# Kernel optimization log

Hardware: AMD Instinct MI355X
Metric: run time of the kernel (lower is better)

Reference implementation:

```python
import jax, jax.numpy as jnp
import numpy as np

B, N, D, H = 1, 4096, 1024, 16
E = D // H  # head_dim = 64


def setup_inputs() -> dict:
    key = jax.random.key(0)
    ks = jax.random.split(key, 5)
    s = 0.02
    return {
        "query": jax.random.normal(ks[0], (B, N, D), dtype=jnp.float32),
        "Wq": jax.random.normal(ks[1], (D, D), dtype=jnp.float32) * s,
        "Wk": jax.random.normal(ks[2], (D, D), dtype=jnp.float32) * s,
        "Wv": jax.random.normal(ks[3], (D, D), dtype=jnp.float32) * s,
        "Wo": jax.random.normal(ks[4], (D, D), dtype=jnp.float32) * s,
        "bo": jnp.zeros((D,), dtype=jnp.float32),
    }


def reference(query, Wq, Wk, Wv, Wo, bo):
    # self-attention: key = value = query
    # nn.Linear: y = x @ W.T  (weights stored as [out, in])
    q = query @ Wq.T  # [b, n, d]
    k = query @ Wk.T
    v = query @ Wv.T
    # 'b n (h e) -> b h n e'
    q = q.reshape(B, N, H, E).transpose(0, 2, 1, 3)
    k = k.reshape(B, N, H, E).transpose(0, 2, 1, 3)
    v = v.reshape(B, N, H, E).transpose(0, 2, 1, 3)
    scale = 1.0 / jnp.sqrt(jnp.asarray(E, dtype=q.dtype))
    attn = jnp.einsum('bhne,bhme->bhnm', q, k) * scale  # [b, h, n, n]
    attn = jax.nn.softmax(attn, axis=-1)
    out = jnp.einsum('bhnm,bhme->bhne', attn, v)  # [b, h, n, e]
    # 'b h n e -> b n (h e)'
    out = out.transpose(0, 2, 1, 3).reshape(B, N, D)
    out = out @ Wo.T + bo
    return out
```

## Files before the change

kernel.cpp:

```cpp
#include <hip/hip_runtime.h>


typedef __attribute__((ext_vector_type(8))) __bf16 bf16x8;
typedef __attribute__((ext_vector_type(4))) float f32x4;
typedef __attribute__((ext_vector_type(16))) float f32x16;
typedef __attribute__((ext_vector_type(4))) unsigned short us4;
typedef __attribute__((ext_vector_type(4))) unsigned int u32x4;
typedef __attribute__((ext_vector_type(2))) unsigned int u32x2;

#define DEV __device__ __forceinline__

#define QSCALE 0.1803368801111204f

DEV unsigned short f2bf(float x) {
  union { float f; unsigned u; } c; c.f = x;
  unsigned u = c.u;
  u += 0x7FFFu + ((u >> 16) & 1u);
  return (unsigned short)(u >> 16);
}

DEV float expq(float x) {
#if __has_builtin(__builtin_amdgcn_exp2f)
  return __builtin_amdgcn_exp2f(x);
#else
  float r;
  asm("v_exp_f32 %0, %1" : "=v"(r) : "v"(x));
  return r;
#endif
}

DEV unsigned cvtpk_bf16(float lo, float hi) {
  unsigned r;
  asm("v_cvt_pk_bf16_f32 %0, %1, %2" : "=v"(r) : "v"(lo), "v"(hi));
  return r;
}

DEV void plswap_u(unsigned& a, unsigned& b) {
#if __has_builtin(__builtin_amdgcn_permlane32_swap)
  u32x2 r = __builtin_amdgcn_permlane32_swap(a, b, false, false);
  a = r.x; b = r.y;
#else
  asm("v_permlane32_swap_b32 %0, %1" : "+v"(a), "+v"(b));
#endif
}

DEV void plswap_f(float& a, float& b) {
  unsigned ua = __float_as_uint(a), ub = __float_as_uint(b);
  plswap_u(ua, ub);
  a = __uint_as_float(ua); b = __uint_as_float(ub);
}

DEV void gload16(const void* g, void* lds) {
  __builtin_amdgcn_global_load_lds(
      (const __attribute__((address_space(1))) unsigned int*)g,
      (__attribute__((address_space(3))) unsigned int*)lds, 16, 0, 0);
}

__global__ void cast_all(const float* __restrict__ q,
                         const float* __restrict__ wa,
                         const float* __restrict__ wb,
                         const float* __restrict__ wc,
                         const float* __restrict__ wd,
                         unsigned short* __restrict__ qo,
                         unsigned short* __restrict__ wout) {
  const int y = blockIdx.y;
  const int i = blockIdx.x * 256 + threadIdx.x;
  const float* src;
  unsigned short* dst;
  if (y < 4) {
    src = q + (size_t)y * 1048576;
    dst = qo + (size_t)y * 1048576;
  } else {
    src = (y == 4) ? wa : (y == 5) ? wb : (y == 6) ? wc : wd;
    dst = wout + (size_t)(y - 4) * 1048576;
  }
  float4 v = reinterpret_cast<const float4*>(src)[i];
  us4 o;
  o.x = f2bf(v.x); o.y = f2bf(v.y); o.z = f2bf(v.z); o.w = f2bf(v.w);
  reinterpret_cast<us4*>(dst)[i] = o;
}

__global__ __launch_bounds__(256)
void gemm_qkv(const unsigned short* __restrict__ A,
              const unsigned short* __restrict__ B,
              unsigned short* __restrict__ Qo,
              unsigned short* __restrict__ Ko,
              unsigned short* __restrict__ Vo) {
  constexpr int K = 1024, BK = 64;
  __shared__ unsigned short As[128 * BK];
  __shared__ unsigned short Bs[128 * BK];
  const int t = threadIdx.x;
  const int w = t >> 6, l = t & 63;
  const int brow = blockIdx.x * 128;
  const int bcol = blockIdx.y * 128;
  const int wr = w >> 1, wc = w & 1;
  const int lr = l >> 3;
  const int lc = ((l & 7) ^ lr) * 8;
  const int fr = l & 15;
  const int fcb = (l >> 4) * 16;
  const int swz = (l & 7) << 4;

  f32x4 acc[4][4] = {};
  const char* Asb = (const char*)As;
  const char* Bsb = (const char*)Bs;

  for (int k0 = 0; k0 < K; k0 += BK) {
#pragma unroll
    for (int i = 0; i < 4; ++i) {
      const int r = w * 32 + i * 8;
      gload16(A + (size_t)(brow + r + lr) * K + k0 + lc, (void*)(As + r * BK));
      gload16(B + (size_t)(bcol + r + lr) * K + k0 + lc, (void*)(Bs + r * BK));
    }
    __syncthreads();
#pragma unroll
    for (int kk = 0; kk < 2; ++kk) {
      bf16x8 af[4], bfr[4];
#pragma unroll
      for (int m = 0; m < 4; ++m)
        af[m] = *(const bf16x8*)(Asb + (wr * 64 + m * 16 + fr) * 128 +
                                 ((kk * 64 + fcb) ^ swz));
#pragma unroll
      for (int n = 0; n < 4; ++n)
        bfr[n] = *(const bf16x8*)(Bsb + (wc * 64 + n * 16 + fr) * 128 +
                                  ((kk * 64 + fcb) ^ swz));
#pragma unroll
      for (int m = 0; m < 4; ++m)
#pragma unroll
        for (int n = 0; n < 4; ++n)
          acc[m][n] = __builtin_amdgcn_mfma_f32_16x16x32_bf16(
              af[m], bfr[n], acc[m][n], 0, 0, 0);
    }
    __syncthreads();
  }

  const int seg = blockIdx.y >> 3;
  const int orow = brow + wr * 64 + (l >> 4) * 4;
  const int ocol = (blockIdx.y & 7) * 128 + wc * 64 + fr;
  if (seg == 1) {
#pragma unroll
    for (int n = 0; n < 4; ++n) {
      const int C = ocol + n * 16;
      const int bn = (C >> 6) * 262144 + ((C & 63) >> 3) * 512 + (C & 7);
#pragma unroll
      for (int m = 0; m < 4; ++m)
#pragma unroll
        for (int j = 0; j < 4; ++j) {
          const int R = orow + m * 16 + j;
          Ko[bn + (R >> 6) * 4096 + (R & 63) * 8] = f2bf(acc[m][n][j]);
        }
    }
  } else if (seg == 2) {
#pragma unroll
    for (int n = 0; n < 4; ++n) {
      const int C = ocol + n * 16;
      const int bn = (C >> 6) * 262144 + (C & 63) * 8;
#pragma unroll
      for (int m = 0; m < 4; ++m)
#pragma unroll
        for (int j = 0; j < 4; ++j) {
          const int R = orow + m * 16 + j;
          Vo[bn + (R >> 6) * 4096 + ((R & 63) >> 3) * 512 + (R & 7)] =
              f2bf(acc[m][n][j]);
        }
    }
  } else {
#pragma unroll
    for (int m = 0; m < 4; ++m)
#pragma unroll
      for (int n = 0; n < 4; ++n)
#pragma unroll
        for (int j = 0; j < 4; ++j)
          Qo[(size_t)(orow + m * 16 + j) * 1024 + (ocol + n * 16)] =
              f2bf(acc[m][n][j] * QSCALE);
  }
}

__global__ __launch_bounds__(256)
void gemm_out64(const unsigned short* __restrict__ A,
                const unsigned short* __restrict__ B,
                float* __restrict__ C, const float* __restrict__ bias) {
  constexpr int N = 1024, K = 1024, BK = 64;
  __shared__ unsigned short As[64 * BK];
  __shared__ unsigned short Bs[128 * BK];
  const int t = threadIdx.x;
  const int w = t >> 6, l = t & 63;
  const int brow = blockIdx.x * 64;
  const int bcol = blockIdx.y * 128;
  const int wr = w >> 1, wc = w & 1;
  const int lr = l >> 3;
  const int lc = ((l & 7) ^ lr) * 8;
  const int fr = l & 15;
  const int fcb = (l >> 4) * 16;
  const int swz = (l & 7) << 4;

  f32x4 acc[2][4] = {};
  const char* Asb = (const char*)As;
  const char* Bsb = (const char*)Bs;

  for (int k0 = 0; k0 < K; k0 += BK) {
#pragma unroll
    for (int i = 0; i < 2; ++i) {
      const int r = w * 16 + i * 8;
      gload16(A + (size_t)(brow + r + lr) * K + k0 + lc, (void*)(As + r * BK));
    }
#pragma unroll
    for (int i = 0; i < 4; ++i) {
      const int r = w * 32 + i * 8;
      gload16(B + (size_t)(bcol + r + lr) * K + k0 + lc, (void*)(Bs + r * BK));
    }
    __syncthreads();
#pragma unroll
    for (int kk = 0; kk < 2; ++kk) {
      bf16x8 af[2], bfr[4];
#pragma unroll
      for (int m = 0; m < 2; ++m)
        af[m] = *(const bf16x8*)(Asb + (wr * 32 + m * 16 + fr) * 128 +
                                 ((kk * 64 + fcb) ^ swz));
#pragma unroll
      for (int n = 0; n < 4; ++n)
        bfr[n] = *(const bf16x8*)(Bsb + (wc * 64 + n * 16 + fr) * 128 +
                                  ((kk * 64 + fcb) ^ swz));
#pragma unroll
      for (int m = 0; m < 2; ++m)
#pragma unroll
        for (int n = 0; n < 4; ++n)
          acc[m][n] = __builtin_amdgcn_mfma_f32_16x16x32_bf16(
              af[m], bfr[n], acc[m][n], 0, 0, 0);
    }
    __syncthreads();
  }

  const int orow = brow + wr * 32 + (l >> 4) * 4;
  const int ocol = bcol + wc * 64 + fr;
#pragma unroll
  for (int m = 0; m < 2; ++m)
#pragma unroll
    for (int n = 0; n < 4; ++n)
#pragma unroll
      for (int j = 0; j < 4; ++j)
        C[(size_t)(orow + m * 16 + j) * N + (ocol + n * 16)] =
            acc[m][n][j] + bias[ocol + n * 16];
}

__global__ __launch_bounds__(512, 4)
void attn_v14(const unsigned short* __restrict__ Q,
              const unsigned short* __restrict__ Kp,
              const unsigned short* __restrict__ Vp,
              unsigned short* __restrict__ AO) {
  constexpr int D = 1024, NIT = 32;
  __shared__ unsigned long long LDSA[65536 / 8];
  char* LDS = (char*)LDSA;
  const int t = threadIdx.x, w = t >> 6, l = t & 63;
  const int g = w >> 2, wg = w & 3;
  const int flat = blockIdx.x;
  const int c = flat & 7, ii = flat >> 3;
  const int h = c * 2 + (ii >> 5);
  const int qt = ii & 31;
  const int q0 = qt * 128 + wg * 32;
  const int ln = l & 31, hi = l >> 5;
  const int lr = l >> 3;
  const int ko = hi * 1024 + ln * 16;

  char* kb0 = LDS + (g * 2 + 0) * 8192;
  char* kb1 = LDS + (g * 2 + 1) * 8192;
  char* vb0 = LDS + 32768 + (g * 2 + 0) * 8192;
  char* vb1 = LDS + 32768 + (g * 2 + 1) * 8192;

  bf16x8 qf[4];
  {
    const unsigned short* qp = Q + (size_t)(q0 + ln) * D + h * 64 + hi * 8;
#pragma unroll
    for (int ks = 0; ks < 4; ++ks) qf[ks] = *(const bf16x8*)(qp + ks * 16);
  }

  f32x16 oacc0 = {}, oacc1 = {};
  float lsum = 0.f;

  const int stoff = wg * 2048;
  const char* Kg = (const char*)Kp + ((size_t)(h * 64 + g)) * 8192 + stoff + l * 16;
  const char* Vg = (const char*)Vp + ((size_t)(h * 64 + g)) * 8192 + stoff + l * 16;

  auto stage = [&](char* kd, char* vd, int it) {
    const size_t o = (size_t)it * 16384;
    gload16(Kg + o, kd + stoff);
    gload16(Kg + o + 1024, kd + stoff + 1024);
    gload16(Vg + o, vd + stoff);
    gload16(Vg + o + 1024, vd + stoff + 1024);
  };

  stage(kb0, vb0, 0);
  __syncthreads();

  for (int i = 0; i < NIT; ++i) {
    const char* ksb = (i & 1) ? kb1 : kb0;
    const char* vsb = (i & 1) ? vb1 : vb0;
    if (i + 1 < NIT)
      stage((i & 1) ? kb0 : kb1, (i & 1) ? vb0 : vb1, i + 1);

    f32x16 sa = {}, sb = {};
    __builtin_amdgcn_s_setprio(1);
#pragma unroll
    for (int ks = 0; ks < 4; ++ks) {
      bf16x8 kf0 = *(const bf16x8*)(ksb + ks * 2048 + ko);
      bf16x8 kf1 = *(const bf16x8*)(ksb + ks * 2048 + 512 + ko);
      sa = __builtin_amdgcn_mfma_f32_32x32x16_bf16(kf0, qf[ks], sa, 0, 0, 0);
      sb = __builtin_amdgcn_mfma_f32_32x32x16_bf16(kf1, qf[ks], sb, 0, 0, 0);
    }
    __builtin_amdgcn_s_setprio(0);

#pragma unroll
    for (int r = 0; r < 16; ++r) { sa[r] = expq(sa[r]); sb[r] = expq(sb[r]); }
    {
      float red[16];
#pragma unroll
      for (int r = 0; r < 16; ++r) red[r] = sa[r] + sb[r];
#pragma unroll
      for (int s = 8; s >= 1; s >>= 1)
#pragma unroll
        for (int r = 0; r < s; ++r) red[r] += red[r + s];
      lsum += red[0];
    }

    unsigned pw[4][4];
#pragma unroll
    for (int kvs = 0; kvs < 4; ++kvs) {
      const f32x16& S = (kvs < 2) ? sa : sb;
      const int rb = (kvs & 1) * 8;
      unsigned A0 = cvtpk_bf16(S[rb + 0], S[rb + 1]);
      unsigned B0 = cvtpk_bf16(S[rb + 4], S[rb + 5]);
      unsigned A1 = cvtpk_bf16(S[rb + 2], S[rb + 3]);
      unsigned B1 = cvtpk_bf16(S[rb + 6], S[rb + 7]);
      plswap_u(A0, B0);
      plswap_u(A1, B1);
      pw[kvs][0] = A0; pw[kvs][1] = A1; pw[kvs][2] = B0; pw[kvs][3] = B1;
    }

    __builtin_amdgcn_s_setprio(1);
#pragma unroll
    for (int kvs = 0; kvs < 4; ++kvs) {
      u32x4 pv = {pw[kvs][0], pw[kvs][1], pw[kvs][2], pw[kvs][3]};
      bf16x8 pf = __builtin_bit_cast(bf16x8, pv);
      bf16x8 vf0 = *(const bf16x8*)(vsb + kvs * 2048 + ko);
      bf16x8 vf1 = *(const bf16x8*)(vsb + kvs * 2048 + 512 + ko);
      oacc0 = __builtin_amdgcn_mfma_f32_32x32x16_bf16(vf0, pf, oacc0, 0, 0, 0);
      oacc1 = __builtin_amdgcn_mfma_f32_32x32x16_bf16(vf1, pf, oacc1, 0, 0, 0);
    }
    __builtin_amdgcn_s_setprio(0);

    __syncthreads();
  }

  float* cb = (float*)LDS;
  float* cl = (float*)(LDS + 32768);
  if (g == 1) {
    float* p = cb + (wg * 64 + l) * 32;
#pragma unroll
    for (int r = 0; r < 16; ++r) { p[r] = oacc0[r]; p[16 + r] = oacc1[r]; }
    cl[wg * 64 + l] = lsum;
  }
  __syncthreads();
  if (g == 0) {
    float* p = cb + (wg * 64 + l) * 32;
#pragma unroll
    for (int r = 0; r < 16; ++r) { oacc0[r] += p[r]; oacc1[r] += p[16 + r]; }
    lsum += cl[wg * 64 + l];
    float sa2 = lsum, sb2 = lsum;
    plswap_f(sa2, sb2);
    const float inv = 1.0f / (sa2 + sb2);

    char* Osc = LDS + 34816 + wg * 4096;
#pragma unroll
    for (int es = 0; es < 2; ++es)
#pragma unroll
      for (int gg = 0; gg < 4; ++gg)
#pragma unroll
        for (int c2 = 0; c2 < 2; ++c2) {
          const f32x16& oa = es == 0 ? oacc0 : oacc1;
          unsigned pk = cvtpk_bf16(oa[gg * 4 + c2 * 2] * inv,
                                   oa[gg * 4 + c2 * 2 + 1] * inv);
          const int col = es * 64 + gg * 16 + hi * 8 + c2 * 4;
          *(unsigned*)(Osc + ln * 128 + (col ^ ((ln & 7) << 4))) = pk;
        }
#pragma unroll
    for (int p2 = 0; p2 < 4; ++p2) {
      const int q = p2 * 8 + lr;
      bf16x8 ov = *(const bf16x8*)(Osc + q * 128 + (((l & 7) ^ lr) << 4));
      *(bf16x8*)(AO + (size_t)(q0 + q) * D + h * 64 + (l & 7) * 8) = ov;
    }
  }
}

extern "C" void kernel_launch(void* const* d_in, const int* in_sizes, int n_in,
                              void* d_out, int out_size, void* d_ws, size_t ws_size,
                              hipStream_t stream) {
  const float* query = (const float*)d_in[0];
  const float* Wq    = (const float*)d_in[1];
  const float* Wk    = (const float*)d_in[2];
  const float* Wv    = (const float*)d_in[3];
  const float* Wo    = (const float*)d_in[4];
  const float* bo    = (const float*)d_in[5];
  float* out = (float*)d_out;

  char* ws = (char*)d_ws;
  const size_t MB = 1024 * 1024;
  unsigned short* Wqkv_b = (unsigned short*)(ws + 0 * MB);
  unsigned short* Wo_b   = (unsigned short*)(ws + 6 * MB);
  unsigned short* Xb     = (unsigned short*)(ws + 8 * MB);
  unsigned short* Qb     = (unsigned short*)(ws + 16 * MB);
  unsigned short* Kb     = (unsigned short*)(ws + 24 * MB);
  unsigned short* Vtb    = (unsigned short*)(ws + 40 * MB);
  unsigned short* AOb    = (unsigned short*)(ws + 32 * MB);

  cast_all<<<dim3(1024, 8), dim3(256), 0, stream>>>(query, Wq, Wk, Wv, Wo,
                                                    Xb, Wqkv_b);

  gemm_qkv<<<dim3(32, 24), dim3(256), 0, stream>>>(Xb, Wqkv_b, Qb, Kb, Vtb);

  attn_v14<<<dim3(512), dim3(512), 0, stream>>>(Qb, Kb, Vtb, AOb);

  gemm_out64<<<dim3(64, 8), dim3(256), 0, stream>>>(AOb, Wo_b, out, bo);
}
```

Measured before the change: 145.6 us.

## Triple-buffer attention K/V tiles with vmcnt waits and vectorize V stores

The attention kernel now processes half-size K/V tiles per iteration (64 iterations instead of 32) through a three-deep LDS ring. Each step waits with s_waitcnt vmcnt and a single barrier, replacing the double buffer with a trailing __syncthreads, so loads are issued two iterations ahead and LDS use drops from 64KB to 50KB. The QKV GEMM epilogue also writes the transposed V output as 4-element vector stores instead of scalar stores. The aim is better overlap of global loads with MFMA work and fewer store instructions, at the cost of more loop iterations and per-iteration barrier overhead with less MFMA work each.

```diff
diff --git a/kernel.cpp b/kernel.cpp
--- a/kernel.cpp
+++ b/kernel.cpp
@@ -155,13 +155,13 @@
       const int C = ocol + n * 16;
       const int bn = (C >> 6) * 262144 + (C & 63) * 8;
 #pragma unroll
-      for (int m = 0; m < 4; ++m)
-#pragma unroll
-        for (int j = 0; j < 4; ++j) {
-          const int R = orow + m * 16 + j;
-          Vo[bn + (R >> 6) * 4096 + ((R & 63) >> 3) * 512 + (R & 7)] =
-              f2bf(acc[m][n][j]);
-        }
+      for (int m = 0; m < 4; ++m) {
+        const int R0 = orow + m * 16;
+        us4 o4;
+        o4.x = f2bf(acc[m][n][0]); o4.y = f2bf(acc[m][n][1]);
+        o4.z = f2bf(acc[m][n][2]); o4.w = f2bf(acc[m][n][3]);
+        *(us4*)(Vo + bn + (R0 >> 6) * 4096 + ((R0 & 63) >> 3) * 512 + (R0 & 7)) = o4;
+      }
     }
   } else {
 #pragma unroll
@@ -243,12 +243,12 @@
 }
 
 __global__ __launch_bounds__(512, 4)
-void attn_v14(const unsigned short* __restrict__ Q,
+void attn_v15(const unsigned short* __restrict__ Q,
               const unsigned short* __restrict__ Kp,
               const unsigned short* __restrict__ Vp,
               unsigned short* __restrict__ AO) {
-  constexpr int D = 1024, NIT = 32;
-  __shared__ unsigned long long LDSA[65536 / 8];
+  constexpr int D = 1024, NIT = 64;
+  __shared__ unsigned long long LDSA[51200 / 8];
   char* LDS = (char*)LDSA;
   const int t = threadIdx.x, w = t >> 6, l = t & 63;
   const int g = w >> 2, wg = w & 3;
@@ -259,12 +259,9 @@
   const int q0 = qt * 128 + wg * 32;
   const int ln = l & 31, hi = l >> 5;
   const int lr = l >> 3;
-  const int ko = hi * 1024 + ln * 16;
-
-  char* kb0 = LDS + (g * 2 + 0) * 8192;
-  char* kb1 = LDS + (g * 2 + 1) * 8192;
-  char* vb0 = LDS + 32768 + (g * 2 + 0) * 8192;
-  char* vb1 = LDS + 32768 + (g * 2 + 1) * 8192;
+
+  char* kgrp = LDS + g * 12288;
+  char* vgrp = LDS + 24576 + g * 12288;
 
   bf16x8 qf[4];
   {
@@ -276,60 +273,63 @@
   f32x16 oacc0 = {}, oacc1 = {};
   float lsum = 0.f;
 
-  const int stoff = wg * 2048;
-  const char* Kg = (const char*)Kp + ((size_t)(h * 64 + g)) * 8192 + stoff + l * 16;
-  const char* Vg = (const char*)Vp + ((size_t)(h * 64 + g)) * 8192 + stoff + l * 16;
-
-  auto stage = [&](char* kd, char* vd, int it) {
-    const size_t o = (size_t)it * 16384;
-    gload16(Kg + o, kd + stoff);
-    gload16(Kg + o + 1024, kd + stoff + 1024);
-    gload16(Vg + o, vd + stoff);
-    gload16(Vg + o + 1024, vd + stoff + 1024);
+  const char* KgL = (const char*)Kp + (size_t)(h * 64) * 8192 + g * 512 +
+                    (wg * 2 + (l >> 5)) * 1024 + (l & 31) * 16;
+  const char* VgL = (const char*)Vp + (size_t)(h * 64) * 8192 + g * 4096 +
+                    wg * 1024 + l * 16;
+  char* kdst = kgrp + wg * 1024;
+  char* vdst = vgrp + wg * 1024;
+
+  auto stage = [&](int buf, int it) {
+    const size_t o = (size_t)it * 8192;
+    gload16(KgL + o, kdst + buf * 4096);
+    gload16(VgL + o, vdst + buf * 4096);
   };
 
-  stage(kb0, vb0, 0);
-  __syncthreads();
+  stage(0, 0);
+  stage(1, 1);
 
   for (int i = 0; i < NIT; ++i) {
-    const char* ksb = (i & 1) ? kb1 : kb0;
-    const char* vsb = (i & 1) ? vb1 : vb0;
-    if (i + 1 < NIT)
-      stage((i & 1) ? kb0 : kb1, (i & 1) ? vb0 : vb1, i + 1);
-
-    f32x16 sa = {}, sb = {};
+    if (i < NIT - 2)
+      asm volatile("s_waitcnt vmcnt(2)" ::: "memory");
+    else
+      asm volatile("s_waitcnt vmcnt(0)" ::: "memory");
+    __builtin_amdgcn_s_barrier();
+    if (i + 2 < NIT) stage((i + 2) % 3, i + 2);
+
+    const char* ksb = kgrp + (i % 3) * 4096;
+    const char* vsb = vgrp + (i % 3) * 4096;
+
+    f32x16 sa = {};
     __builtin_amdgcn_s_setprio(1);
 #pragma unroll
     for (int ks = 0; ks < 4; ++ks) {
-      bf16x8 kf0 = *(const bf16x8*)(ksb + ks * 2048 + ko);
-      bf16x8 kf1 = *(const bf16x8*)(ksb + ks * 2048 + 512 + ko);
-      sa = __builtin_amdgcn_mfma_f32_32x32x16_bf16(kf0, qf[ks], sa, 0, 0, 0);
-      sb = __builtin_amdgcn_mfma_f32_32x32x16_bf16(kf1, qf[ks], sb, 0, 0, 0);
+      bf16x8 kf = *(const bf16x8*)(ksb + (2 * ks + hi) * 512 + ln * 16);
+      sa = __builtin_amdgcn_mfma_f32_32x32x16_bf16(kf, qf[ks], sa, 0, 0, 0);
     }
     __builtin_amdgcn_s_setprio(0);
 
 #pragma unroll
-    for (int r = 0; r < 16; ++r) { sa[r] = expq(sa[r]); sb[r] = expq(sb[r]); }
+    for (int r = 0; r < 16; ++r) sa[r] = expq(sa[r]);
     {
-      float red[16];
-#pragma unroll
-      for (int r = 0; r < 16; ++r) red[r] = sa[r] + sb[r];
-#pragma unroll
-      for (int s = 8; s >= 1; s >>= 1)
+      float red[8];
+#pragma unroll
+      for (int r = 0; r < 8; ++r) red[r] = sa[r] + sa[r + 8];
+#pragma unroll
+      for (int s = 4; s >= 1; s >>= 1)
 #pragma unroll
         for (int r = 0; r < s; ++r) red[r] += red[r + s];
       lsum += red[0];
     }
 
-    unsigned pw[4][4];
-#pragma unroll
-    for (int kvs = 0; kvs < 4; ++kvs) {
-      const f32x16& S = (kvs < 2) ? sa : sb;
-      const int rb = (kvs & 1) * 8;
-      unsigned A0 = cvtpk_bf16(S[rb + 0], S[rb + 1]);
-      unsigned B0 = cvtpk_bf16(S[rb + 4], S[rb + 5]);
-      unsigned A1 = cvtpk_bf16(S[rb + 2], S[rb + 3]);
-      unsigned B1 = cvtpk_bf16(S[rb + 6], S[rb + 7]);
+    unsigned pw[2][4];
+#pragma unroll
+    for (int kvs = 0; kvs < 2; ++kvs) {
+      const int rb = kvs * 8;
+      unsigned A0 = cvtpk_bf16(sa[rb + 0], sa[rb + 1]);
+      unsigned B0 = cvtpk_bf16(sa[rb + 4], sa[rb + 5]);
+      unsigned A1 = cvtpk_bf16(sa[rb + 2], sa[rb + 3]);
+      unsigned B1 = cvtpk_bf16(sa[rb + 6], sa[rb + 7]);
       plswap_u(A0, B0);
       plswap_u(A1, B1);
       pw[kvs][0] = A0; pw[kvs][1] = A1; pw[kvs][2] = B0; pw[kvs][3] = B1;
@@ -337,18 +337,18 @@
 
     __builtin_amdgcn_s_setprio(1);
 #pragma unroll
-    for (int kvs = 0; kvs < 4; ++kvs) {
+    for (int kvs = 0; kvs < 2; ++kvs) {
       u32x4 pv = {pw[kvs][0], pw[kvs][1], pw[kvs][2], pw[kvs][3]};
       bf16x8 pf = __builtin_bit_cast(bf16x8, pv);
-      bf16x8 vf0 = *(const bf16x8*)(vsb + kvs * 2048 + ko);
-      bf16x8 vf1 = *(const bf16x8*)(vsb + kvs * 2048 + 512 + ko);
+      bf16x8 vf0 = *(const bf16x8*)(vsb + (2 * kvs + hi) * 1024 + ln * 16);
+      bf16x8 vf1 = *(const bf16x8*)(vsb + (2 * kvs + hi) * 1024 + 512 + ln * 16);
       oacc0 = __builtin_amdgcn_mfma_f32_32x32x16_bf16(vf0, pf, oacc0, 0, 0, 0);
       oacc1 = __builtin_amdgcn_mfma_f32_32x32x16_bf16(vf1, pf, oacc1, 0, 0, 0);
     }
     __builtin_amdgcn_s_setprio(0);
-
-    __syncthreads();
-  }
+  }
+
+  __syncthreads();
 
   float* cb = (float*)LDS;
   float* cl = (float*)(LDS + 32768);
@@ -416,7 +416,7 @@
 
   gemm_qkv<<<dim3(32, 24), dim3(256), 0, stream>>>(Xb, Wqkv_b, Qb, Kb, Vtb);
 
-  attn_v14<<<dim3(512), dim3(512), 0, stream>>>(Qb, Kb, Vtb, AOb);
+  attn_v15<<<dim3(512), dim3(512), 0, stream>>>(Qb, Kb, Vtb, AOb);
 
   gemm_out64<<<dim3(64, 8), dim3(256), 0, stream>>>(AOb, Wo_b, out, bo);
 }
```

Result: no change. 145.7 us (+0.0%).
